# Performance work log

Measured on AMD Instinct MI355X. Metric: run time of the kernel, lower is better.

The kernel has to match this reference:

```python
import jax, jax.numpy as jnp
import numpy as np

DIM = 256
NUM_HEADS = 4
HEAD_DIM = DIM // NUM_HEADS


def setup_inputs() -> dict:
    key = jax.random.key(0)
    ks = jax.random.split(key, 8)
    B, N, C = 4, 2048, DIM
    x = jax.random.normal(ks[0], (B, N, C), dtype=jnp.float32)
    R = jax.random.normal(ks[1], (B, 3, 3), dtype=jnp.float32)
    P = jax.random.normal(ks[2], (N, 3), dtype=jnp.float32)
    s = 1.0 / np.sqrt(C)
    qkv_w = jax.random.normal(ks[3], (3 * C, C), dtype=jnp.float32) * s
    qkv_b = jax.random.normal(ks[4], (3 * C,), dtype=jnp.float32) * 0.02
    proj_w = jax.random.normal(ks[5], (C, C), dtype=jnp.float32) * s
    proj_b = jax.random.normal(ks[6], (C,), dtype=jnp.float32) * 0.02
    pos_scale = jnp.asarray(1.0, dtype=jnp.float32)
    return {"x": x, "R": R, "P": P, "qkv_w": qkv_w, "qkv_b": qkv_b,
            "proj_w": proj_w, "proj_b": proj_b, "pos_scale": pos_scale}


def reference(x, R, P, qkv_w, qkv_b, proj_w, proj_b, pos_scale):
    B, N, C = x.shape
    H, D = NUM_HEADS, HEAD_DIM
    scale = D ** -0.5
    # qkv: (B,N,3C) -> (3,B,H,N,D)
    qkv = (x @ qkv_w.T + qkv_b).reshape(B, N, 3, H, D).transpose(2, 0, 3, 1, 4)
    q, k, v = qkv[0], qkv[1], qkv[2]
    # attention logits (B,H,N,N)
    attn = jnp.einsum('bhid,bhjd->bhij', q, k) * scale
    # positional bias: RP = (R @ P^T)^T -> (B,N,3); bias_ij = dot(RP_i, P_j)
    RP = jnp.einsum('bab,jb->bja', R, P) if False else jnp.einsum('bca,ja->bjc', jnp.swapaxes(R, 1, 2), P)
    RP = jnp.einsum('bcd,jd->bjc', R, P)  # (B,N,3): (R @ P.T).T
    bias = jnp.einsum('bik,jk->bij', RP, P)[:, None, :, :] * pos_scale  # (B,1,N,N) broadcast over heads
    attn = jax.nn.softmax(attn + bias, axis=-1)
    out = jnp.einsum('bhij,bhjd->bhid', attn, v)  # (B,H,N,D)
    out = out.transpose(0, 2, 1, 3).reshape(B, N, C)
    out = out @ proj_w.T + proj_b
    return out
```

## Files before the change

### kernel.cpp

```cpp
#include <hip/hip_runtime.h>
#include <hip/hip_bf16.h>

#define B_ 4
#define N_ 2048
#define C_ 256
#define H_ 4
#define D_ 64

typedef __attribute__((ext_vector_type(8))) short bf16x8;
typedef __attribute__((ext_vector_type(4))) float f32x4;

#define LOG2E 1.4426950408889634f

static __device__ inline unsigned short f2bf(float f) {
    unsigned u = __builtin_bit_cast(unsigned, f);
    unsigned r = (u + 0x7fffu + ((u >> 16) & 1u)) >> 16;
    return (unsigned short)r;
}
static __device__ inline float bf2f(unsigned short h) {
    unsigned u = ((unsigned)h) << 16;
    return __builtin_bit_cast(float, u);
}
static __device__ inline unsigned pack2(float a, float b) {
    __hip_bfloat162 h = __float22bfloat162_rn(make_float2(a, b));
    unsigned u;
    __builtin_memcpy(&u, &h, 4);
    return u;
}
static __device__ inline bf16x8 ld_frag(const unsigned short* p) {
    return __builtin_bit_cast(bf16x8, *(const uint4*)p);
}

__global__ __launch_bounds__(256) void prep_kernel(
    const float* __restrict__ x, const float* __restrict__ qkv_w,
    const float* __restrict__ proj_w, const float* __restrict__ Pm,
    unsigned short* __restrict__ xb, unsigned short* __restrict__ wqb,
    unsigned short* __restrict__ wpb, unsigned short* __restrict__ Pext)
{
    const int bid = blockIdx.x, tid = threadIdx.x;
    const float* s; unsigned short* d; int i;
    if (bid < 1024)      { s = x;      d = xb;  i = (bid * 256 + tid) * 8; }
    else if (bid < 1120) { s = qkv_w;  d = wqb; i = ((bid - 1024) * 256 + tid) * 8; }
    else if (bid < 1152) { s = proj_w; d = wpb; i = ((bid - 1120) * 256 + tid) * 8; }
    else {
        int n = (bid - 1152) * 256 + tid;
        if (n >= N_) return;
        unsigned short row[32];
        #pragma unroll
        for (int q = 0; q < 32; ++q) row[q] = 0;
        #pragma unroll
        for (int c = 0; c < 3; ++c) {
            float p = Pm[n * 3 + c];
            unsigned short u = f2bf(p);
            unsigned short v = f2bf(p - bf2f(u));
            row[c] = u; row[3 + c] = v; row[6 + c] = u;
        }
        #pragma unroll
        for (int q = 0; q < 4; ++q)
            *(uint4*)&Pext[(size_t)n * 32 + q * 8] = *(const uint4*)&row[q * 8];
        return;
    }
    float4 a = *(const float4*)(s + i);
    float4 b = *(const float4*)(s + i + 4);
    uint4 u;
    u.x = pack2(a.x, a.y); u.y = pack2(a.z, a.w);
    u.z = pack2(b.x, b.y); u.w = pack2(b.z, b.w);
    *(uint4*)(d + i) = u;
}

__global__ __launch_bounds__(256) void qkv_gemm(
    const unsigned short* __restrict__ xb, const unsigned short* __restrict__ wb,
    const float* __restrict__ bias, unsigned short* __restrict__ qb,
    unsigned short* __restrict__ kb, unsigned short* __restrict__ vt)
{
    __shared__ __align__(16) unsigned short As[128 * 40];
    __shared__ __align__(16) unsigned short Bs[64 * 40];
    const int m0 = blockIdx.x * 128, o0 = blockIdx.y * 64;
    const int tid = threadIdx.x;
    const int wave = tid >> 6, lane = tid & 63, quad = lane >> 4, l16 = lane & 15;

    f32x4 acc[2][4];
    #pragma unroll
    for (int i = 0; i < 2; ++i)
        #pragma unroll
        for (int j = 0; j < 4; ++j) acc[i][j] = (f32x4){0.f, 0.f, 0.f, 0.f};

    for (int k0 = 0; k0 < 256; k0 += 32) {
        __syncthreads();
        {
            int row = tid >> 1, cb = (tid & 1) * 16;
            const unsigned short* src = &xb[(size_t)(m0 + row) * 256 + k0 + cb];
            *(uint4*)&As[row * 40 + cb + 0] = *(const uint4*)(src + 0);
            *(uint4*)&As[row * 40 + cb + 8] = *(const uint4*)(src + 8);
        }
        {
            int row = tid >> 2, cb = (tid & 3) * 8;
            *(uint4*)&Bs[row * 40 + cb] = *(const uint4*)&wb[(size_t)(o0 + row) * 256 + k0 + cb];
        }
        __syncthreads();
        bf16x8 a[2], b[4];
        #pragma unroll
        for (int mt = 0; mt < 2; ++mt) a[mt] = ld_frag(&As[(wave * 32 + mt * 16 + l16) * 40 + quad * 8]);
        #pragma unroll
        for (int nt = 0; nt < 4; ++nt) b[nt] = ld_frag(&Bs[(nt * 16 + l16) * 40 + quad * 8]);
        #pragma unroll
        for (int mt = 0; mt < 2; ++mt)
            #pragma unroll
            for (int nt = 0; nt < 4; ++nt)
                acc[mt][nt] = __builtin_amdgcn_mfma_f32_16x16x32_bf16(a[mt], b[nt], acc[mt][nt], 0, 0, 0);
    }

    const int three = o0 >> 8;
    const int h = (o0 >> 6) & 3;
    const int b = m0 >> 11;
    float bv[4];
    #pragma unroll
    for (int nt = 0; nt < 4; ++nt) bv[nt] = bias[o0 + nt * 16 + l16];

    if (three == 2) {
        const int n64 = ((m0 + (wave >> 1) * 64) & 2047);
        const size_t bh64 = ((size_t)b * H_ + h) * 64;
        #pragma unroll
        for (int nt = 0; nt < 4; ++nt) {
            int d = nt * 16 + l16;
            #pragma unroll
            for (int r = 0; r < 4; ++r) {
                unsigned pw = pack2(acc[0][nt][r] + bv[nt], acc[1][nt][r] + bv[nt]);
                *(unsigned*)&vt[(bh64 + d) * N_ + n64 + 16 * quad + 4 * r + 2 * (wave & 1)] = pw;
            }
        }
    } else {
        unsigned short* dst = (three == 0) ? qb : kb;
        float sc = (three == 0) ? (0.125f * LOG2E) : 1.0f;
        #pragma unroll
        for (int mt = 0; mt < 2; ++mt)
            #pragma unroll
            for (int r = 0; r < 4; ++r) {
                int m = m0 + wave * 32 + mt * 16 + quad * 4 + r;
                int n = m & 2047;
                size_t rowbase = (((size_t)b * H_ + h) * N_ + n) * D_;
                #pragma unroll
                for (int nt = 0; nt < 4; ++nt)
                    dst[rowbase + nt * 16 + l16] = f2bf((acc[mt][nt][r] + bv[nt]) * sc);
            }
    }
}

#define LDK 72
#define LDKX 104

__global__ __launch_bounds__(256) void attn_kernel(
    const unsigned short* __restrict__ qb, const unsigned short* __restrict__ kb,
    const unsigned short* __restrict__ vt, const unsigned short* __restrict__ Pext,
    const float* __restrict__ Rm, const float* __restrict__ Pm,
    const float* __restrict__ ps_ptr,
    unsigned short* __restrict__ Opart, float* __restrict__ ml)
{
    __shared__ __align__(16) unsigned short Ks[64 * LDKX];
    __shared__ __align__(16) unsigned short Vs[64 * LDK];
    __shared__ __align__(16) unsigned short Ps[64 * LDK];

    const int bh = blockIdx.y;
    const int b = bh >> 2;
    const int i0 = blockIdx.x * 64;
    const int split = blockIdx.z;
    const int tid = threadIdx.x;
    const int wave = tid >> 6, lane = tid & 63;
    const int quad = lane >> 4, l16 = lane & 15;
    const float ps = ps_ptr[0];

    const size_t base = (size_t)bh * N_ * D_;
    const unsigned short* qg = qb + base;
    const unsigned short* kg = kb + base;
    const unsigned short* vg = vt + base;

    const int qrow = i0 + wave * 16 + l16;
    bf16x8 aq[3];
    #pragma unroll
    for (int ks = 0; ks < 2; ++ks)
        aq[ks] = ld_frag(&qg[(size_t)qrow * D_ + ks * 32 + quad * 8]);

    {
        float p0 = Pm[qrow * 3 + 0], p1 = Pm[qrow * 3 + 1], p2 = Pm[qrow * 3 + 2];
        float sc = ps * LOG2E;
        unsigned short ah[3], al[3];
        #pragma unroll
        for (int c = 0; c < 3; ++c) {
            float a = (Rm[b * 9 + c * 3 + 0] * p0 + Rm[b * 9 + c * 3 + 1] * p1
                     + Rm[b * 9 + c * 3 + 2] * p2) * sc;
            ah[c] = f2bf(a);
            al[c] = f2bf(a - bf2f(ah[c]));
        }
        bf16x8 e = (bf16x8){0,0,0,0,0,0,0,0};
        if (quad == 0) {
            e[0] = (short)ah[0]; e[1] = (short)ah[1]; e[2] = (short)ah[2];
            e[3] = (short)ah[0]; e[4] = (short)ah[1]; e[5] = (short)ah[2];
            e[6] = (short)al[0]; e[7] = (short)al[1];
        } else if (quad == 1) {
            e[0] = (short)al[2];
        }
        aq[2] = e;
    }

    const bf16x8 ones = (bf16x8){0x3F80,0x3F80,0x3F80,0x3F80,0x3F80,0x3F80,0x3F80,0x3F80};

    float m_run = -1e30f;
    f32x4 o_acc[4], lacc;
    #pragma unroll
    for (int t = 0; t < 4; ++t) o_acc[t] = (f32x4){0.f, 0.f, 0.f, 0.f};
    lacc = (f32x4){0.f, 0.f, 0.f, 0.f};

    const int jbeg = split * (N_ / 2);
    for (int jt = 0; jt < (N_ / 2) / 64; ++jt) {
        const int j0 = jbeg + jt * 64;
        __syncthreads();
        #pragma unroll
        for (int rr = 0; rr < 2; ++rr) {
            int c = tid + rr * 256;
            int row = c >> 3, off = (c & 7) * 8;
            *(uint4*)&Ks[row * LDKX + off] = *(const uint4*)&kg[(size_t)(j0 + row) * D_ + off];
            *(uint4*)&Vs[row * LDK + off] = *(const uint4*)&vg[(size_t)row * N_ + j0 + off];
        }
        {
            int row = tid >> 2, q4 = tid & 3;
            *(uint4*)&Ks[row * LDKX + 64 + q4 * 8] = *(const uint4*)&Pext[(size_t)(j0 + row) * 32 + q4 * 8];
        }
        __syncthreads();

        f32x4 s[4];
        #pragma unroll
        for (int t = 0; t < 4; ++t) {
            f32x4 c = {0.f, 0.f, 0.f, 0.f};
            #pragma unroll
            for (int ks = 0; ks < 3; ++ks) {
                bf16x8 bk = ld_frag(&Ks[(l16 + 16 * t) * LDKX + ks * 32 + quad * 8]);
                c = __builtin_amdgcn_mfma_f32_16x16x32_bf16(aq[ks], bk, c, 0, 0, 0);
            }
            s[t] = c;
        }

        float mx = m_run;
        #pragma unroll
        for (int t = 0; t < 4; ++t)
            #pragma unroll
            for (int r = 0; r < 4; ++r)
                mx = fmaxf(mx, s[t][r]);
        #pragma unroll
        for (int off = 1; off < 64; off <<= 1)
            mx = fmaxf(mx, __shfl_xor(mx, off));
        const float alpha = exp2f(m_run - mx);
        m_run = mx;

        #pragma unroll
        for (int r = 0; r < 4; ++r) {
            float p0 = exp2f(s[0][r] - mx), p1 = exp2f(s[1][r] - mx);
            float p2 = exp2f(s[2][r] - mx), p3 = exp2f(s[3][r] - mx);
            uint2 w;
            w.x = pack2(p0, p1);
            w.y = pack2(p2, p3);
            *(uint2*)&Ps[(wave * 16 + quad * 4 + r) * LDK + 4 * l16] = w;
        }

        #pragma unroll
        for (int t = 0; t < 4; ++t)
            #pragma unroll
            for (int r = 0; r < 4; ++r)
                o_acc[t][r] *= alpha;
        #pragma unroll
        for (int r = 0; r < 4; ++r) lacc[r] *= alpha;

        #pragma unroll
        for (int ks = 0; ks < 2; ++ks) {
            bf16x8 ap = ld_frag(&Ps[(wave * 16 + l16) * LDK + ks * 32 + quad * 8]);
            #pragma unroll
            for (int t = 0; t < 4; ++t) {
                bf16x8 bv = ld_frag(&Vs[(l16 + 16 * t) * LDK + ks * 32 + quad * 8]);
                o_acc[t] = __builtin_amdgcn_mfma_f32_16x16x32_bf16(ap, bv, o_acc[t], 0, 0, 0);
            }
            lacc = __builtin_amdgcn_mfma_f32_16x16x32_bf16(ap, ones, lacc, 0, 0, 0);
        }
    }

    const size_t pbase = (size_t)(split * 16 + bh) * N_;
    #pragma unroll
    for (int r = 0; r < 4; ++r) {
        int row = i0 + wave * 16 + quad * 4 + r;
        #pragma unroll
        for (int t = 0; t < 4; ++t)
            Opart[(pbase + row) * D_ + l16 + 16 * t] = f2bf(o_acc[t][r]);
        if (l16 == 0) {
            float2* mlp = (float2*)ml;
            mlp[pbase + row] = make_float2(m_run, lacc[r]);
        }
    }
}

__global__ __launch_bounds__(256) void proj_gemm(
    const unsigned short* __restrict__ Opart, const float* __restrict__ ml,
    const unsigned short* __restrict__ wb, const float* __restrict__ bias,
    float* __restrict__ out)
{
    __shared__ __align__(16) unsigned short As[64 * 40];
    __shared__ __align__(16) unsigned short Bs[64 * 40];
    const int m0 = blockIdx.x * 64, o0 = blockIdx.y * 64;
    const int tid = threadIdx.x;
    const int wave = tid >> 6, lane = tid & 63, quad = lane >> 4, l16 = lane & 15;
    const float2* mlp = (const float2*)ml;

    f32x4 acc[4];
    #pragma unroll
    for (int j = 0; j < 4; ++j) acc[j] = (f32x4){0.f, 0.f, 0.f, 0.f};

    for (int k0 = 0; k0 < 256; k0 += 32) {
        __syncthreads();
        {
            int row = tid >> 2, cb = (tid & 3) * 8;
            int m = m0 + row;
            int b = m >> 11, n = m & 2047;
            int h = k0 >> 6, d0 = (k0 & 63) + cb;
            size_t r1 = (size_t)(b * 4 + h) * N_ + n;
            size_t r2 = (size_t)(16 + b * 4 + h) * N_ + n;
            float2 ml1 = mlp[r1], ml2 = mlp[r2];
            float mm = fmaxf(ml1.x, ml2.x);
            float w1 = exp2f(ml1.x - mm), w2 = exp2f(ml2.x - mm);
            float inv = 1.f / (ml1.y * w1 + ml2.y * w2);
            w1 *= inv; w2 *= inv;
            union { uint4 u; unsigned short s[8]; } a1, a2;
            a1.u = *(const uint4*)&Opart[r1 * D_ + d0];
            a2.u = *(const uint4*)&Opart[r2 * D_ + d0];
            uint4 mv;
            unsigned* mp = (unsigned*)&mv;
            #pragma unroll
            for (int j = 0; j < 4; ++j)
                mp[j] = pack2(bf2f(a1.s[2*j]) * w1 + bf2f(a2.s[2*j]) * w2,
                              bf2f(a1.s[2*j+1]) * w1 + bf2f(a2.s[2*j+1]) * w2);
            *(uint4*)&As[row * 40 + cb] = mv;
        }
        {
            int row = tid >> 2, cb = (tid & 3) * 8;
            *(uint4*)&Bs[row * 40 + cb] = *(const uint4*)&wb[(size_t)(o0 + row) * 256 + k0 + cb];
        }
        __syncthreads();
        bf16x8 a = ld_frag(&As[(wave * 16 + l16) * 40 + quad * 8]);
        #pragma unroll
        for (int nt = 0; nt < 4; ++nt) {
            bf16x8 b = ld_frag(&Bs[(nt * 16 + l16) * 40 + quad * 8]);
            acc[nt] = __builtin_amdgcn_mfma_f32_16x16x32_bf16(a, b, acc[nt], 0, 0, 0);
        }
    }

    float bv[4];
    #pragma unroll
    for (int nt = 0; nt < 4; ++nt) bv[nt] = bias[o0 + nt * 16 + l16];
    #pragma unroll
    for (int r = 0; r < 4; ++r) {
        int m = m0 + wave * 16 + quad * 4 + r;
        #pragma unroll
        for (int nt = 0; nt < 4; ++nt)
            out[(size_t)m * 256 + o0 + nt * 16 + l16] = acc[nt][r] + bv[nt];
    }
}

extern "C" void kernel_launch(void* const* d_in, const int* in_sizes, int n_in,
                              void* d_out, int out_size, void* d_ws, size_t ws_size,
                              hipStream_t stream) {
    const float* x       = (const float*)d_in[0];
    const float* Rm      = (const float*)d_in[1];
    const float* Pm      = (const float*)d_in[2];
    const float* qkv_w   = (const float*)d_in[3];
    const float* qkv_b   = (const float*)d_in[4];
    const float* proj_w  = (const float*)d_in[5];
    const float* proj_b  = (const float*)d_in[6];
    const float* pos_scl = (const float*)d_in[7];
    float* out = (float*)d_out;

    const size_t NE = (size_t)B_ * H_ * N_ * D_;
    unsigned short* xb    = (unsigned short*)d_ws;
    unsigned short* wqb   = xb   + NE;
    unsigned short* wpb   = wqb  + 768 * 256;
    unsigned short* pext  = wpb  + 256 * 256;
    unsigned short* qb    = pext + 2048 * 32;
    unsigned short* kb    = qb   + NE;
    unsigned short* vtb   = kb   + NE;
    unsigned short* opart = vtb  + NE;
    float*          mlb   = (float*)(opart + 2 * NE);

    prep_kernel<<<1160, 256, 0, stream>>>(x, qkv_w, proj_w, Pm, xb, wqb, wpb, pext);
    qkv_gemm<<<dim3(64, 12), 256, 0, stream>>>(xb, wqb, qkv_b, qb, kb, vtb);
    attn_kernel<<<dim3(32, 16, 2), 256, 0, stream>>>(qb, kb, vtb, pext, Rm, Pm, pos_scl, opart, mlb);
    proj_gemm<<<dim3(128, 4), 256, 0, stream>>>(opart, mlb, wpb, proj_b, out);
}
```

Baseline: 147.8 us.

## Register-prefetch next tiles in QKV, attention, and projection kernels

Adds software prefetching through registers in all three GEMM/attention loops: the next K/V/Pext or A/B tile is loaded from global memory into registers right after the shared-memory barrier, so the load overlaps the current tile's MFMA work. The projection kernel also computes the split-softmax merge weights once per head up front instead of every k-step. The online-softmax rescale is skipped when alpha equals one, and pack2 now uses a manual rounding helper. The trade-off is extra register pressure from the held prefetch values and a small branch in the inner loop.

Measured after the change: 148.8 us. About the same (+0.7%).

```diff
diff --git a/kernel.cpp b/kernel.cpp
--- a/kernel.cpp
+++ b/kernel.cpp
@@ -22,10 +22,7 @@
     return __builtin_bit_cast(float, u);
 }
 static __device__ inline unsigned pack2(float a, float b) {
-    __hip_bfloat162 h = __float22bfloat162_rn(make_float2(a, b));
-    unsigned u;
-    __builtin_memcpy(&u, &h, 4);
-    return u;
+    return (unsigned)f2bf(a) | ((unsigned)f2bf(b) << 16);
 }
 static __device__ inline bf16x8 ld_frag(const unsigned short* p) {
     return __builtin_bit_cast(bf16x8, *(const uint4*)p);
@@ -85,19 +82,29 @@
         #pragma unroll
         for (int j = 0; j < 4; ++j) acc[i][j] = (f32x4){0.f, 0.f, 0.f, 0.f};
 
+    const int arow = tid >> 1, acb = (tid & 1) * 16;
+    const int brow = tid >> 2, bcb = (tid & 3) * 8;
+
+    uint4 ra0, ra1, rb;
+    {
+        const unsigned short* s = &xb[(size_t)(m0 + arow) * 256 + acb];
+        ra0 = *(const uint4*)(s);
+        ra1 = *(const uint4*)(s + 8);
+        rb = *(const uint4*)&wb[(size_t)(o0 + brow) * 256 + bcb];
+    }
+
     for (int k0 = 0; k0 < 256; k0 += 32) {
         __syncthreads();
-        {
-            int row = tid >> 1, cb = (tid & 1) * 16;
-            const unsigned short* src = &xb[(size_t)(m0 + row) * 256 + k0 + cb];
-            *(uint4*)&As[row * 40 + cb + 0] = *(const uint4*)(src + 0);
-            *(uint4*)&As[row * 40 + cb + 8] = *(const uint4*)(src + 8);
-        }
-        {
-            int row = tid >> 2, cb = (tid & 3) * 8;
-            *(uint4*)&Bs[row * 40 + cb] = *(const uint4*)&wb[(size_t)(o0 + row) * 256 + k0 + cb];
-        }
-        __syncthreads();
+        *(uint4*)&As[arow * 40 + acb + 0] = ra0;
+        *(uint4*)&As[arow * 40 + acb + 8] = ra1;
+        *(uint4*)&Bs[brow * 40 + bcb] = rb;
+        __syncthreads();
+        if (k0 + 32 < 256) {
+            const unsigned short* s = &xb[(size_t)(m0 + arow) * 256 + k0 + 32 + acb];
+            ra0 = *(const uint4*)(s);
+            ra1 = *(const uint4*)(s + 8);
+            rb = *(const uint4*)&wb[(size_t)(o0 + brow) * 256 + k0 + 32 + bcb];
+        }
         bf16x8 a[2], b[4];
         #pragma unroll
         for (int mt = 0; mt < 2; ++mt) a[mt] = ld_frag(&As[(wave * 32 + mt * 16 + l16) * 40 + quad * 8]);
@@ -211,21 +218,38 @@
     lacc = (f32x4){0.f, 0.f, 0.f, 0.f};
 
     const int jbeg = split * (N_ / 2);
-    for (int jt = 0; jt < (N_ / 2) / 64; ++jt) {
-        const int j0 = jbeg + jt * 64;
-        __syncthreads();
-        #pragma unroll
-        for (int rr = 0; rr < 2; ++rr) {
-            int c = tid + rr * 256;
-            int row = c >> 3, off = (c & 7) * 8;
-            *(uint4*)&Ks[row * LDKX + off] = *(const uint4*)&kg[(size_t)(j0 + row) * D_ + off];
-            *(uint4*)&Vs[row * LDK + off] = *(const uint4*)&vg[(size_t)row * N_ + j0 + off];
-        }
-        {
-            int row = tid >> 2, q4 = tid & 3;
-            *(uint4*)&Ks[row * LDKX + 64 + q4 * 8] = *(const uint4*)&Pext[(size_t)(j0 + row) * 32 + q4 * 8];
-        }
-        __syncthreads();
+    const int NT = (N_ / 2) / 64;
+    const int srow = tid >> 3, soff = (tid & 7) * 8;
+    const int srow2 = srow + 32;
+    const int perow = tid >> 2, peq = (tid & 3) * 8;
+
+    uint4 rk0, rk1, rv0, rv1, rpe;
+    {
+        const int j0 = jbeg;
+        rk0 = *(const uint4*)&kg[(size_t)(j0 + srow) * D_ + soff];
+        rk1 = *(const uint4*)&kg[(size_t)(j0 + srow2) * D_ + soff];
+        rv0 = *(const uint4*)&vg[(size_t)srow * N_ + j0 + soff];
+        rv1 = *(const uint4*)&vg[(size_t)srow2 * N_ + j0 + soff];
+        rpe = *(const uint4*)&Pext[(size_t)(j0 + perow) * 32 + peq];
+    }
+
+    for (int jt = 0; jt < NT; ++jt) {
+        __syncthreads();
+        *(uint4*)&Ks[srow * LDKX + soff] = rk0;
+        *(uint4*)&Ks[srow2 * LDKX + soff] = rk1;
+        *(uint4*)&Vs[srow * LDK + soff] = rv0;
+        *(uint4*)&Vs[srow2 * LDK + soff] = rv1;
+        *(uint4*)&Ks[perow * LDKX + 64 + peq] = rpe;
+        __syncthreads();
+
+        if (jt + 1 < NT) {
+            const int j0n = jbeg + (jt + 1) * 64;
+            rk0 = *(const uint4*)&kg[(size_t)(j0n + srow) * D_ + soff];
+            rk1 = *(const uint4*)&kg[(size_t)(j0n + srow2) * D_ + soff];
+            rv0 = *(const uint4*)&vg[(size_t)srow * N_ + j0n + soff];
+            rv1 = *(const uint4*)&vg[(size_t)srow2 * N_ + j0n + soff];
+            rpe = *(const uint4*)&Pext[(size_t)(j0n + perow) * 32 + peq];
+        }
 
         f32x4 s[4];
         #pragma unroll
@@ -261,13 +285,15 @@
             *(uint2*)&Ps[(wave * 16 + quad * 4 + r) * LDK + 4 * l16] = w;
         }
 
-        #pragma unroll
-        for (int t = 0; t < 4; ++t)
-            #pragma unroll
-            for (int r = 0; r < 4; ++r)
-                o_acc[t][r] *= alpha;
-        #pragma unroll
-        for (int r = 0; r < 4; ++r) lacc[r] *= alpha;
+        if (alpha < 1.0f) {
+            #pragma unroll
+            for (int t = 0; t < 4; ++t)
+                #pragma unroll
+                for (int r = 0; r < 4; ++r)
+                    o_acc[t][r] *= alpha;
+            #pragma unroll
+            for (int r = 0; r < 4; ++r) lacc[r] *= alpha;
+        }
 
         #pragma unroll
         for (int ks = 0; ks < 2; ++ks) {
@@ -307,40 +333,56 @@
     const int wave = tid >> 6, lane = tid & 63, quad = lane >> 4, l16 = lane & 15;
     const float2* mlp = (const float2*)ml;
 
+    const int srow = tid >> 2, scb = (tid & 3) * 8;
+    const int sm = m0 + srow, sb = sm >> 11, sn = sm & 2047;
+
+    float w1h[4], w2h[4];
+    #pragma unroll
+    for (int h = 0; h < 4; ++h) {
+        size_t r1 = (size_t)(sb * 4 + h) * N_ + sn;
+        float2 ml1 = mlp[r1], ml2 = mlp[r1 + 16 * N_];
+        float mm = fmaxf(ml1.x, ml2.x);
+        float w1 = exp2f(ml1.x - mm), w2 = exp2f(ml2.x - mm);
+        float inv = 1.f / (ml1.y * w1 + ml2.y * w2);
+        w1h[h] = w1 * inv; w2h[h] = w2 * inv;
+    }
+
     f32x4 acc[4];
     #pragma unroll
     for (int j = 0; j < 4; ++j) acc[j] = (f32x4){0.f, 0.f, 0.f, 0.f};
 
+    uint4 rA1, rA2, rB;
+    {
+        size_t r1 = (size_t)(sb * 4 + 0) * N_ + sn;
+        rA1 = *(const uint4*)&Opart[r1 * D_ + scb];
+        rA2 = *(const uint4*)&Opart[(r1 + 16 * N_) * D_ + scb];
+        rB = *(const uint4*)&wb[(size_t)(o0 + srow) * 256 + scb];
+    }
+
     for (int k0 = 0; k0 < 256; k0 += 32) {
+        const int h = k0 >> 6;
         __syncthreads();
         {
-            int row = tid >> 2, cb = (tid & 3) * 8;
-            int m = m0 + row;
-            int b = m >> 11, n = m & 2047;
-            int h = k0 >> 6, d0 = (k0 & 63) + cb;
-            size_t r1 = (size_t)(b * 4 + h) * N_ + n;
-            size_t r2 = (size_t)(16 + b * 4 + h) * N_ + n;
-            float2 ml1 = mlp[r1], ml2 = mlp[r2];
-            float mm = fmaxf(ml1.x, ml2.x);
-            float w1 = exp2f(ml1.x - mm), w2 = exp2f(ml2.x - mm);
-            float inv = 1.f / (ml1.y * w1 + ml2.y * w2);
-            w1 *= inv; w2 *= inv;
+            float w1 = w1h[h], w2 = w2h[h];
             union { uint4 u; unsigned short s[8]; } a1, a2;
-            a1.u = *(const uint4*)&Opart[r1 * D_ + d0];
-            a2.u = *(const uint4*)&Opart[r2 * D_ + d0];
+            a1.u = rA1; a2.u = rA2;
             uint4 mv;
             unsigned* mp = (unsigned*)&mv;
             #pragma unroll
             for (int j = 0; j < 4; ++j)
                 mp[j] = pack2(bf2f(a1.s[2*j]) * w1 + bf2f(a2.s[2*j]) * w2,
                               bf2f(a1.s[2*j+1]) * w1 + bf2f(a2.s[2*j+1]) * w2);
-            *(uint4*)&As[row * 40 + cb] = mv;
-        }
-        {
-            int row = tid >> 2, cb = (tid & 3) * 8;
-            *(uint4*)&Bs[row * 40 + cb] = *(const uint4*)&wb[(size_t)(o0 + row) * 256 + k0 + cb];
-        }
-        __syncthreads();
+            *(uint4*)&As[srow * 40 + scb] = mv;
+            *(uint4*)&Bs[srow * 40 + scb] = rB;
+        }
+        __syncthreads();
+        if (k0 + 32 < 256) {
+            const int hn = (k0 + 32) >> 6, d0n = ((k0 + 32) & 63) + scb;
+            size_t r1 = (size_t)(sb * 4 + hn) * N_ + sn;
+            rA1 = *(const uint4*)&Opart[r1 * D_ + d0n];
+            rA2 = *(const uint4*)&Opart[(r1 + 16 * N_) * D_ + d0n];
+            rB = *(const uint4*)&wb[(size_t)(o0 + srow) * 256 + k0 + 32 + scb];
+        }
         bf16x8 a = ld_frag(&As[(wave * 16 + l16) * 40 + quad * 8]);
         #pragma unroll
         for (int nt = 0; nt < 4; ++nt) {
```

## Fuse bf16 conversion into GEMMs, build P extension in-kernel, split attention 4-way

Applied to the files above, without the earlier changes.

Removes the separate prep kernel: the QKV and projection GEMMs now load fp32 inputs and weights and pack them to bf16 while staging into shared memory. The attention kernel builds the P hi/lo extension rows itself from P instead of reading a precomputed buffer. The key-dimension split grows from 2 to 4, so the projection GEMM now merges four partial outputs with log-sum-exp weights that are precomputed once per row. Rescaling of the running accumulators is also skipped when alpha equals 1. The aim is to cut one launch and its extra memory traffic and to raise attention parallelism, at the cost of more partial-output traffic and redundant conversion work in the GEMMs.

Result: no change. 148.9 us (+0.7%).

```diff
diff --git a/kernel.cpp b/kernel.cpp
--- a/kernel.cpp
+++ b/kernel.cpp
@@ -27,49 +27,18 @@
     __builtin_memcpy(&u, &h, 4);
     return u;
 }
-static __device__ inline bf16x8 ld_frag(const unsigned short* p) {
-    return __builtin_bit_cast(bf16x8, *(const uint4*)p);
-}
-
-__global__ __launch_bounds__(256) void prep_kernel(
-    const float* __restrict__ x, const float* __restrict__ qkv_w,
-    const float* __restrict__ proj_w, const float* __restrict__ Pm,
-    unsigned short* __restrict__ xb, unsigned short* __restrict__ wqb,
-    unsigned short* __restrict__ wpb, unsigned short* __restrict__ Pext)
-{
-    const int bid = blockIdx.x, tid = threadIdx.x;
-    const float* s; unsigned short* d; int i;
-    if (bid < 1024)      { s = x;      d = xb;  i = (bid * 256 + tid) * 8; }
-    else if (bid < 1120) { s = qkv_w;  d = wqb; i = ((bid - 1024) * 256 + tid) * 8; }
-    else if (bid < 1152) { s = proj_w; d = wpb; i = ((bid - 1120) * 256 + tid) * 8; }
-    else {
-        int n = (bid - 1152) * 256 + tid;
-        if (n >= N_) return;
-        unsigned short row[32];
-        #pragma unroll
-        for (int q = 0; q < 32; ++q) row[q] = 0;
-        #pragma unroll
-        for (int c = 0; c < 3; ++c) {
-            float p = Pm[n * 3 + c];
-            unsigned short u = f2bf(p);
-            unsigned short v = f2bf(p - bf2f(u));
-            row[c] = u; row[3 + c] = v; row[6 + c] = u;
-        }
-        #pragma unroll
-        for (int q = 0; q < 4; ++q)
-            *(uint4*)&Pext[(size_t)n * 32 + q * 8] = *(const uint4*)&row[q * 8];
-        return;
-    }
-    float4 a = *(const float4*)(s + i);
-    float4 b = *(const float4*)(s + i + 4);
+static __device__ inline uint4 pk8(float4 a, float4 b) {
     uint4 u;
     u.x = pack2(a.x, a.y); u.y = pack2(a.z, a.w);
     u.z = pack2(b.x, b.y); u.w = pack2(b.z, b.w);
-    *(uint4*)(d + i) = u;
+    return u;
+}
+static __device__ inline bf16x8 ld_frag(const unsigned short* p) {
+    return __builtin_bit_cast(bf16x8, *(const uint4*)p);
 }
 
 __global__ __launch_bounds__(256) void qkv_gemm(
-    const unsigned short* __restrict__ xb, const unsigned short* __restrict__ wb,
+    const float* __restrict__ x, const float* __restrict__ w,
     const float* __restrict__ bias, unsigned short* __restrict__ qb,
     unsigned short* __restrict__ kb, unsigned short* __restrict__ vt)
 {
@@ -85,17 +54,23 @@
         #pragma unroll
         for (int j = 0; j < 4; ++j) acc[i][j] = (f32x4){0.f, 0.f, 0.f, 0.f};
 
+    const int arow = tid >> 1, acb = (tid & 1) * 16;
+    const int brow = tid >> 2, bcb = (tid & 3) * 8;
+    const float* asrc = &x[(size_t)(m0 + arow) * 256 + acb];
+    const float* bsrc = &w[(size_t)(o0 + brow) * 256 + bcb];
+
     for (int k0 = 0; k0 < 256; k0 += 32) {
         __syncthreads();
         {
-            int row = tid >> 1, cb = (tid & 1) * 16;
-            const unsigned short* src = &xb[(size_t)(m0 + row) * 256 + k0 + cb];
-            *(uint4*)&As[row * 40 + cb + 0] = *(const uint4*)(src + 0);
-            *(uint4*)&As[row * 40 + cb + 8] = *(const uint4*)(src + 8);
-        }
-        {
-            int row = tid >> 2, cb = (tid & 3) * 8;
-            *(uint4*)&Bs[row * 40 + cb] = *(const uint4*)&wb[(size_t)(o0 + row) * 256 + k0 + cb];
+            float4 a0 = *(const float4*)(asrc + k0);
+            float4 a1 = *(const float4*)(asrc + k0 + 4);
+            float4 a2 = *(const float4*)(asrc + k0 + 8);
+            float4 a3 = *(const float4*)(asrc + k0 + 12);
+            float4 b0 = *(const float4*)(bsrc + k0);
+            float4 b1 = *(const float4*)(bsrc + k0 + 4);
+            *(uint4*)&As[arow * 40 + acb + 0] = pk8(a0, a1);
+            *(uint4*)&As[arow * 40 + acb + 8] = pk8(a2, a3);
+            *(uint4*)&Bs[brow * 40 + bcb] = pk8(b0, b1);
         }
         __syncthreads();
         bf16x8 a[2], b[4];
@@ -151,7 +126,7 @@
 
 __global__ __launch_bounds__(256) void attn_kernel(
     const unsigned short* __restrict__ qb, const unsigned short* __restrict__ kb,
-    const unsigned short* __restrict__ vt, const unsigned short* __restrict__ Pext,
+    const unsigned short* __restrict__ vt,
     const float* __restrict__ Rm, const float* __restrict__ Pm,
     const float* __restrict__ ps_ptr,
     unsigned short* __restrict__ Opart, float* __restrict__ ml)
@@ -174,6 +149,12 @@
     const unsigned short* kg = kb + base;
     const unsigned short* vg = vt + base;
 
+    if (tid < 64) {
+        uint4 z = {0u, 0u, 0u, 0u};
+        *(uint4*)&Ks[tid * LDKX + 80] = z;
+        *(uint4*)&Ks[tid * LDKX + 88] = z;
+    }
+
     const int qrow = i0 + wave * 16 + l16;
     bf16x8 aq[3];
     #pragma unroll
@@ -210,8 +191,10 @@
     for (int t = 0; t < 4; ++t) o_acc[t] = (f32x4){0.f, 0.f, 0.f, 0.f};
     lacc = (f32x4){0.f, 0.f, 0.f, 0.f};
 
-    const int jbeg = split * (N_ / 2);
-    for (int jt = 0; jt < (N_ / 2) / 64; ++jt) {
+    const int jbeg = split * (N_ / 4);
+    const int NT = (N_ / 4) / 64;
+
+    for (int jt = 0; jt < NT; ++jt) {
         const int j0 = jbeg + jt * 64;
         __syncthreads();
         #pragma unroll
@@ -221,9 +204,19 @@
             *(uint4*)&Ks[row * LDKX + off] = *(const uint4*)&kg[(size_t)(j0 + row) * D_ + off];
             *(uint4*)&Vs[row * LDK + off] = *(const uint4*)&vg[(size_t)row * N_ + j0 + off];
         }
-        {
-            int row = tid >> 2, q4 = tid & 3;
-            *(uint4*)&Ks[row * LDKX + 64 + q4 * 8] = *(const uint4*)&Pext[(size_t)(j0 + row) * 32 + q4 * 8];
+        if (tid < 64) {
+            const float* pp = &Pm[(size_t)(j0 + tid) * 3];
+            float p0 = pp[0], p1 = pp[1], p2 = pp[2];
+            unsigned u0 = f2bf(p0), u1 = f2bf(p1), u2 = f2bf(p2);
+            unsigned v0 = f2bf(p0 - bf2f((unsigned short)u0));
+            unsigned v1 = f2bf(p1 - bf2f((unsigned short)u1));
+            unsigned v2 = f2bf(p2 - bf2f((unsigned short)u2));
+            uint4 lo, hi;
+            lo.x = u0 | (u1 << 16); lo.y = u2 | (v0 << 16);
+            lo.z = v1 | (v2 << 16); lo.w = u0 | (u1 << 16);
+            hi.x = u2; hi.y = 0u; hi.z = 0u; hi.w = 0u;
+            *(uint4*)&Ks[tid * LDKX + 64] = lo;
+            *(uint4*)&Ks[tid * LDKX + 72] = hi;
         }
         __syncthreads();
 
@@ -261,13 +254,15 @@
             *(uint2*)&Ps[(wave * 16 + quad * 4 + r) * LDK + 4 * l16] = w;
         }
 
-        #pragma unroll
-        for (int t = 0; t < 4; ++t)
-            #pragma unroll
-            for (int r = 0; r < 4; ++r)
-                o_acc[t][r] *= alpha;
-        #pragma unroll
-        for (int r = 0; r < 4; ++r) lacc[r] *= alpha;
+        if (alpha < 1.0f) {
+            #pragma unroll
+            for (int t = 0; t < 4; ++t)
+                #pragma unroll
+                for (int r = 0; r < 4; ++r)
+                    o_acc[t][r] *= alpha;
+            #pragma unroll
+            for (int r = 0; r < 4; ++r) lacc[r] *= alpha;
+        }
 
         #pragma unroll
         for (int ks = 0; ks < 2; ++ks) {
@@ -297,7 +292,7 @@
 
 __global__ __launch_bounds__(256) void proj_gemm(
     const unsigned short* __restrict__ Opart, const float* __restrict__ ml,
-    const unsigned short* __restrict__ wb, const float* __restrict__ bias,
+    const float* __restrict__ w, const float* __restrict__ bias,
     float* __restrict__ out)
 {
     __shared__ __align__(16) unsigned short As[64 * 40];
@@ -307,38 +302,53 @@
     const int wave = tid >> 6, lane = tid & 63, quad = lane >> 4, l16 = lane & 15;
     const float2* mlp = (const float2*)ml;
 
+    const int srow = tid >> 2, scb = (tid & 3) * 8;
+    const int sm = m0 + srow, sb = sm >> 11, sn = sm & 2047;
+
+    float wgt[4][4];
+    #pragma unroll
+    for (int h = 0; h < 4; ++h) {
+        size_t r1 = (size_t)(sb * 4 + h) * N_ + sn;
+        float2 m0v = mlp[r1], m1v = mlp[r1 + 16 * N_];
+        float2 m2v = mlp[r1 + 32 * N_], m3v = mlp[r1 + 48 * N_];
+        float mm = fmaxf(fmaxf(m0v.x, m1v.x), fmaxf(m2v.x, m3v.x));
+        float w0 = exp2f(m0v.x - mm), w1 = exp2f(m1v.x - mm);
+        float w2 = exp2f(m2v.x - mm), w3 = exp2f(m3v.x - mm);
+        float inv = 1.f / (m0v.y * w0 + m1v.y * w1 + m2v.y * w2 + m3v.y * w3);
+        wgt[h][0] = w0 * inv; wgt[h][1] = w1 * inv;
+        wgt[h][2] = w2 * inv; wgt[h][3] = w3 * inv;
+    }
+
     f32x4 acc[4];
     #pragma unroll
     for (int j = 0; j < 4; ++j) acc[j] = (f32x4){0.f, 0.f, 0.f, 0.f};
 
     for (int k0 = 0; k0 < 256; k0 += 32) {
+        const int h = k0 >> 6;
+        const int d0 = (k0 & 63) + scb;
         __syncthreads();
         {
-            int row = tid >> 2, cb = (tid & 3) * 8;
-            int m = m0 + row;
-            int b = m >> 11, n = m & 2047;
-            int h = k0 >> 6, d0 = (k0 & 63) + cb;
-            size_t r1 = (size_t)(b * 4 + h) * N_ + n;
-            size_t r2 = (size_t)(16 + b * 4 + h) * N_ + n;
-            float2 ml1 = mlp[r1], ml2 = mlp[r2];
-            float mm = fmaxf(ml1.x, ml2.x);
-            float w1 = exp2f(ml1.x - mm), w2 = exp2f(ml2.x - mm);
-            float inv = 1.f / (ml1.y * w1 + ml2.y * w2);
-            w1 *= inv; w2 *= inv;
-            union { uint4 u; unsigned short s[8]; } a1, a2;
-            a1.u = *(const uint4*)&Opart[r1 * D_ + d0];
-            a2.u = *(const uint4*)&Opart[r2 * D_ + d0];
+            size_t r1 = (size_t)(sb * 4 + h) * N_ + sn;
+            union { uint4 u; unsigned short s[8]; } a0, a1, a2, a3;
+            a0.u = *(const uint4*)&Opart[r1 * D_ + d0];
+            a1.u = *(const uint4*)&Opart[(r1 + 16 * N_) * D_ + d0];
+            a2.u = *(const uint4*)&Opart[(r1 + 32 * N_) * D_ + d0];
+            a3.u = *(const uint4*)&Opart[(r1 + 48 * N_) * D_ + d0];
+            float w0 = wgt[h][0], w1 = wgt[h][1], w2 = wgt[h][2], w3 = wgt[h][3];
             uint4 mv;
             unsigned* mp = (unsigned*)&mv;
             #pragma unroll
-            for (int j = 0; j < 4; ++j)
-                mp[j] = pack2(bf2f(a1.s[2*j]) * w1 + bf2f(a2.s[2*j]) * w2,
-                              bf2f(a1.s[2*j+1]) * w1 + bf2f(a2.s[2*j+1]) * w2);
-            *(uint4*)&As[row * 40 + cb] = mv;
-        }
-        {
-            int row = tid >> 2, cb = (tid & 3) * 8;
-            *(uint4*)&Bs[row * 40 + cb] = *(const uint4*)&wb[(size_t)(o0 + row) * 256 + k0 + cb];
+            for (int j = 0; j < 4; ++j) {
+                float lo = bf2f(a0.s[2*j]) * w0 + bf2f(a1.s[2*j]) * w1
+                         + bf2f(a2.s[2*j]) * w2 + bf2f(a3.s[2*j]) * w3;
+                float hi = bf2f(a0.s[2*j+1]) * w0 + bf2f(a1.s[2*j+1]) * w1
+                         + bf2f(a2.s[2*j+1]) * w2 + bf2f(a3.s[2*j+1]) * w3;
+                mp[j] = pack2(lo, hi);
+            }
+            *(uint4*)&As[srow * 40 + scb] = mv;
+            float4 b0 = *(const float4*)&w[(size_t)(o0 + srow) * 256 + k0 + scb];
+            float4 b1 = *(const float4*)&w[(size_t)(o0 + srow) * 256 + k0 + scb + 4];
+            *(uint4*)&Bs[srow * 40 + scb] = pk8(b0, b1);
         }
         __syncthreads();
         bf16x8 a = ld_frag(&As[(wave * 16 + l16) * 40 + quad * 8]);
@@ -375,18 +385,13 @@
     float* out = (float*)d_out;
 
     const size_t NE = (size_t)B_ * H_ * N_ * D_;
-    unsigned short* xb    = (unsigned short*)d_ws;
-    unsigned short* wqb   = xb   + NE;
-    unsigned short* wpb   = wqb  + 768 * 256;
-    unsigned short* pext  = wpb  + 256 * 256;
-    unsigned short* qb    = pext + 2048 * 32;
-    unsigned short* kb    = qb   + NE;
-    unsigned short* vtb   = kb   + NE;
-    unsigned short* opart = vtb  + NE;
-    float*          mlb   = (float*)(opart + 2 * NE);
-
-    prep_kernel<<<1160, 256, 0, stream>>>(x, qkv_w, proj_w, Pm, xb, wqb, wpb, pext);
-    qkv_gemm<<<dim3(64, 12), 256, 0, stream>>>(xb, wqb, qkv_b, qb, kb, vtb);
-    attn_kernel<<<dim3(32, 16, 2), 256, 0, stream>>>(qb, kb, vtb, pext, Rm, Pm, pos_scl, opart, mlb);
-    proj_gemm<<<dim3(128, 4), 256, 0, stream>>>(opart, mlb, wpb, proj_b, out);
-}
+    unsigned short* qb    = (unsigned short*)d_ws;
+    unsigned short* kb    = qb  + NE;
+    unsigned short* vtb   = kb  + NE;
+    unsigned short* opart = vtb + NE;
+    float*          mlb   = (float*)(opart + 4 * NE);
+
+    qkv_gemm<<<dim3(64, 12), 256, 0, stream>>>(x, qkv_w, qkv_b, qb, kb, vtb);
+    attn_kernel<<<dim3(32, 16, 4), 256, 0, stream>>>(qb, kb, vtb, Rm, Pm, pos_scl, opart, mlb);
+    proj_gemm<<<dim3(128, 4), 256, 0, stream>>>(opart, mlb, proj_w, proj_b, out);
+}
```
